# Kernel optimization log

Measured on AMD Instinct MI355X. Metric: run time of the kernel, lower is better.

Reference implementation:

```python
import jax, jax.numpy as jnp
import numpy as np
from jax import lax

RADII = (0.1, 0.2, 0.4)
NSAMPLES = (16, 32, 128)
MLPS = ((3, 32, 32, 64), (3, 64, 64, 128), (3, 64, 96, 128))  # divide_ratio=1


def fps(xyz, npoint):
    # iterative farthest point sampling; xyz [B,N,3] -> idx [B,npoint]
    B, N, _ = xyz.shape
    def body(carry, _):
        mind, last = carry
        p = jnp.take_along_axis(xyz, last[:, None, None], axis=1)  # [B,1,3]
        d = jnp.sum((xyz - p) ** 2, -1)
        mind = jnp.minimum(mind, d)
        nxt = jnp.argmax(mind, -1).astype(jnp.int32)
        return (mind, nxt), last
    init = (jnp.full((B, N), 1e10, xyz.dtype), jnp.zeros((B,), jnp.int32))
    _, idx = lax.scan(body, init, None, length=npoint)
    return jnp.transpose(idx)  # [B,npoint]


def ball_query(radius, nsample, xyz, new_xyz):
    # first-nsample neighbors within radius; pad with first valid index
    N = xyz.shape[1]
    sq = jnp.sum((new_xyz[:, :, None, :] - xyz[:, None, :, :]) ** 2, -1)  # [B,S,N]
    cand = jnp.where(sq < radius * radius,
                     jnp.arange(N, dtype=jnp.int32)[None, None, :], N)
    idx = jnp.sort(cand, axis=-1)[:, :, :nsample]
    first = idx[:, :, :1]
    return jnp.where(idx == N, first, idx).astype(jnp.int32)


def scale_branch(xyz, new_xyz, radius, nsample, weights):
    idx = ball_query(radius, nsample, xyz, new_xyz)
    grouped = jax.vmap(lambda x, i: x[i])(xyz, idx)          # [B,S,ns,3]
    h = grouped - new_xyz[:, :, None, :]                      # relative coords (points=None)
    for w, b in weights:                                      # shared 1x1-conv MLP
        h = jax.nn.relu(jnp.einsum('bsnc,co->bsno', h, w) + b)
    return jnp.max(h, axis=2)                                 # maxpool over neighbors [B,S,C]


def _forward(pcd, params, wf, bf):
    npoint = pcd.shape[1] // 8
    idx = fps(pcd, npoint)
    new_xyz = jnp.take_along_axis(pcd, idx[:, :, None], axis=1)  # [B,S,3]
    feats = [scale_branch(pcd, new_xyz, RADII[i], NSAMPLES[i], params[i]) for i in range(3)]
    h = jnp.concatenate(feats, axis=-1)                          # [B,S,320]
    return jnp.einsum('bsc,co->bso', h, wf) + bf                 # patch values [B,S,1]


def setup_inputs() -> dict:
    key = jax.random.key(0)
    ks = jax.random.split(key, 32)
    B, N = 8, 4096
    inp = {"pcd": jax.random.uniform(ks[0], (B, N, 3), jnp.float32)}
    ki = 1
    for si, dims in enumerate(MLPS):
        for li in range(3):
            cin, cout = dims[li], dims[li + 1]
            inp[f"w{si}{li}"] = jax.random.normal(ks[ki], (cin, cout), jnp.float32) * (2.0 / cin) ** 0.5
            inp[f"b{si}{li}"] = jnp.zeros((cout,), jnp.float32)
            ki += 1
    inp["wf"] = jax.random.normal(ks[ki], (320, 1), jnp.float32) * 0.05
    inp["bf"] = jnp.zeros((1,), jnp.float32)
    return inp


def reference(pcd, w00, b00, w01, b01, w02, b02,
              w10, b10, w11, b11, w12, b12,
              w20, b20, w21, b21, w22, b22, wf, bf):
    params = [[(w00, b00), (w01, b01), (w02, b02)],
              [(w10, b10), (w11, b11), (w12, b12)],
              [(w20, b20), (w21, b21), (w22, b22)]]
    return _forward(pcd, params, wf, bf)
```

## Files before the change

kernel.cpp:

```cpp
#include <hip/hip_runtime.h>

#define BATCH 8
#define NPTS 4096
#define NSAMP 512

#define ROW_SHR(n) (0x110 | (n))
#define ROW_BCAST15 0x142
#define ROW_BCAST31 0x143

typedef __attribute__((ext_vector_type(8))) short bf16x8;
typedef __attribute__((ext_vector_type(4))) float f32x4;

__device__ __forceinline__ unsigned short f2bf(float f) {
  unsigned u = __float_as_uint(f);
  unsigned r = (u + 0x7FFFu + ((u >> 16) & 1u)) >> 16;
  return (unsigned short)r;
}
__device__ __forceinline__ float bf2f(unsigned short h) {
  return __uint_as_float(((unsigned)h) << 16);
}

template <int CTRL, int RMASK>
__device__ __forceinline__ float fmax_dpp(float x) {
  int t = __builtin_amdgcn_update_dpp(0, __float_as_int(x), CTRL, RMASK, 0xf, true);
  return fmaxf(x, __int_as_float(t));
}

__device__ __forceinline__ float wave_max(float x) {
  x = fmax_dpp<ROW_SHR(1), 0xf>(x);
  x = fmax_dpp<ROW_SHR(2), 0xf>(x);
  x = fmax_dpp<ROW_SHR(4), 0xf>(x);
  x = fmax_dpp<ROW_SHR(8), 0xf>(x);
  x = fmax_dpp<ROW_BCAST15, 0xa>(x);
  x = fmax_dpp<ROW_BCAST31, 0xc>(x);
  return x;
}

__device__ __forceinline__ void tsec(int g, const float* __restrict__ w,
                                     float* __restrict__ wt, int cin, int cinp,
                                     int cout, int base) {
  int local = g - base;
  if (local < 0 || local >= cinp * cout) return;
  int oc = local / cinp, ic = local % cinp;
  wt[base + local] = (ic < cin) ? w[ic * cout + oc] : 0.0f;
}

__device__ __forceinline__ void rowpack(int g, const float* __restrict__ w20,
                                        const float* __restrict__ b20,
                                        const float* __restrict__ w21,
                                        float* __restrict__ wt, int base) {
  int local = g - base;
  if (local < 0 || local >= 4 * 64 * 32) return;
  int wq = local / (64 * 32);
  int r = local % (64 * 32);
  int k = r / 32, j = r % 32;
  float v;
  if (j < 3) v = w20[j * 64 + k];
  else if (j == 3) v = b20[k];
  else if (j < 28) v = w21[k * 96 + wq * 24 + (j - 4)];
  else v = 0.0f;
  wt[base + local] = v;
}

__device__ __forceinline__ void awfill(int g, const float* __restrict__ w22,
                                       unsigned short* __restrict__ aw,
                                       int base) {
  int id = g - base;
  if (id < 0 || id >= 12288) return;
  int e = id & 7;
  int l = (id >> 3) & 63;
  int bq = id >> 9;
  int ot = bq / 3, ks = bq % 3;
  int oc = ot * 16 + (l & 15);
  int k = ks * 32 + (l >> 4) * 8 + e;
  float v = w22[k * 128 + oc];
  unsigned short h = f2bf(v);
  unsigned short lo = f2bf(__fsub_rn(v, bf2f(h)));
  aw[(bq * 64 + l) * 16 + e] = h;
  aw[(bq * 64 + l) * 16 + 8 + e] = lo;
}

#define W00 0
#define W01 128
#define W02 1152
#define W10 3200
#define W11 3456
#define W12 7552
#define WROW 15744
#define AWID 23936
#define ID_TOTAL 36224

__global__ __launch_bounds__(256) void prep_kernel(
    const float* w00, const float* w01, const float* w02,
    const float* w10, const float* w11, const float* w12,
    const float* w20, const float* b20, const float* w21, const float* w22,
    float* __restrict__ wt, unsigned short* __restrict__ aw) {
  int g = blockIdx.x * 256 + threadIdx.x;
  tsec(g, w00, wt, 3, 4, 32, W00);
  tsec(g, w01, wt, 32, 32, 32, W01);
  tsec(g, w02, wt, 32, 32, 64, W02);
  tsec(g, w10, wt, 3, 4, 64, W10);
  tsec(g, w11, wt, 64, 64, 64, W11);
  tsec(g, w12, wt, 64, 64, 128, W12);
  rowpack(g, w20, b20, w21, wt, WROW);
  awfill(g, w22, aw, AWID);
}

template <int TOC, int TN>
__device__ __forceinline__ void ib(float (&acc)[TOC][TN], const float* bias) {
#pragma unroll
  for (int j = 0; j < TOC; ++j) {
    float bj = bias[j];
#pragma unroll
    for (int i = 0; i < TN; ++i) acc[j][i] = bj;
  }
}

template <int CIN4, int TOC, int TN, int NTPI, int WS>
__device__ __forceinline__ void layer_acc(const float* __restrict__ wtb,
                                          const float* hin,
                                          float (&acc)[TOC][TN], int tn) {
#pragma unroll 2
  for (int c4 = 0; c4 < CIN4; ++c4) {
    float hv[4][TN];
#pragma unroll
    for (int k = 0; k < 4; ++k) {
      const float* src = &hin[(c4 * 4 + k) * NTPI + tn * TN];
      if constexpr (TN == 1) {
        hv[k][0] = src[0];
      } else if constexpr (TN == 2) {
        float2 v = *(const float2*)src; hv[k][0] = v.x; hv[k][1] = v.y;
      } else {
        float4 v = *(const float4*)src;
        hv[k][0] = v.x; hv[k][1] = v.y; hv[k][2] = v.z; hv[k][3] = v.w;
      }
    }
#pragma unroll
    for (int j = 0; j < TOC; ++j) {
      float4 w4 = *(const float4*)&wtb[j * WS + c4 * 4];
#pragma unroll
      for (int i = 0; i < TN; ++i) {
        acc[j][i] = fmaf(hv[0][i], w4.x, acc[j][i]);
        acc[j][i] = fmaf(hv[1][i], w4.y, acc[j][i]);
        acc[j][i] = fmaf(hv[2][i], w4.z, acc[j][i]);
        acc[j][i] = fmaf(hv[3][i], w4.w, acc[j][i]);
      }
    }
  }
}

template <int TOC, int TN, int NTPO>
__device__ __forceinline__ void store_relu(float* hout,
                                           float (&acc)[TOC][TN], int tn) {
#pragma unroll
  for (int j = 0; j < TOC; ++j) {
    float* dst = &hout[j * NTPO + tn * TN];
    if constexpr (TN == 1) {
      dst[0] = fmaxf(acc[j][0], 0.0f);
    } else if constexpr (TN == 2) {
      *(float2*)dst = make_float2(fmaxf(acc[j][0], 0.0f),
                                  fmaxf(acc[j][1], 0.0f));
    } else {
      *(float4*)dst = make_float4(fmaxf(acc[j][0], 0.0f),
                                  fmaxf(acc[j][1], 0.0f),
                                  fmaxf(acc[j][2], 0.0f),
                                  fmaxf(acc[j][3], 0.0f));
    }
  }
}

template <int TOC, int TN>
__device__ __forceinline__ float rmax_dot(const float* wfp,
                                          float (&acc)[TOC][TN], int tn) {
  float s = 0.0f;
#pragma unroll
  for (int j = 0; j < TOC; ++j) {
    float v = 0.0f;
#pragma unroll
    for (int i = 0; i < TN; ++i) v = fmaxf(v, acc[j][i]);
    v = fmaxf(v, __shfl_xor(v, 1));
    v = fmaxf(v, __shfl_xor(v, 2));
    v = fmaxf(v, __shfl_xor(v, 4));
    v = fmaxf(v, __shfl_xor(v, 8));
    if (tn == 0) s = fmaf(v, wfp[j], s);
  }
  return s;
}

__global__ __launch_bounds__(256) void fused_kernel(
    const float* __restrict__ pcd, float* __restrict__ new_xyz,
    int* __restrict__ ctrl, const float* __restrict__ wt,
    const unsigned short* __restrict__ aw,
    const float* __restrict__ b00, const float* __restrict__ b01,
    const float* __restrict__ b02, const float* __restrict__ b10,
    const float* __restrict__ b11, const float* __restrict__ b12,
    const float* __restrict__ b21, const float* __restrict__ b22,
    const float* __restrict__ wf, const float* __restrict__ bf,
    float* __restrict__ out) {
  __shared__ __align__(16) float lds[6160];

  const int tid = threadIdx.x;
  int* progress = ctrl + 8;

  if (tid == 0) ((int*)lds)[0] = atomicAdd(&ctrl[0], 1);
  __syncthreads();
  const int ticket = ((int*)lds)[0];

  if (ticket < BATCH) {
    const int b = ticket;
    const int t = tid;
    const int wave = t >> 6, lane = t & 63;
    const float* xb = pcd + (size_t)b * NPTS * 3;
    float4* slot = (float4*)(lds + 16);

    float X[16], Y[16], Z[16], mind[16];
    {
      float f[48];
      float4* vv = (float4*)f;
      const float4* src = (const float4*)xb + t * 12;
#pragma unroll
      for (int q = 0; q < 12; ++q) vv[q] = src[q];
#pragma unroll
      for (int j = 0; j < 16; ++j) {
        X[j] = f[3 * j + 0]; Y[j] = f[3 * j + 1]; Z[j] = f[3 * j + 2];
        mind[j] = 10000000000.0f;
      }
    }
    float px = xb[0], py = xb[1], pz = xb[2];

    for (int it = 0; it < NSAMP; ++it) {
      if (t == 0) {
        int* dst = (int*)(new_xyz + ((size_t)b * NSAMP + it) * 3);
        atomicExch(&dst[0], __float_as_int(px));
        atomicExch(&dst[1], __float_as_int(py));
        atomicExch(&dst[2], __float_as_int(pz));
        if ((it & 7) == 7)
          __hip_atomic_store(&progress[b], it + 1, __ATOMIC_RELEASE,
                             __HIP_MEMORY_SCOPE_AGENT);
      }
      float bv = -1.0f, bx = 0.0f, by = 0.0f, bz = 0.0f;
#pragma unroll
      for (int j = 0; j < 16; ++j) {
        float dx = __fsub_rn(X[j], px);
        float dy = __fsub_rn(Y[j], py);
        float dz = __fsub_rn(Z[j], pz);
        float d = __fadd_rn(__fadd_rn(__fmul_rn(dx, dx), __fmul_rn(dy, dy)),
                            __fmul_rn(dz, dz));
        float m = fminf(mind[j], d);
        mind[j] = m;
        bool g = m > bv;
        bv = g ? m : bv;
        bx = g ? X[j] : bx; by = g ? Y[j] : by; bz = g ? Z[j] : bz;
      }
      float wmax = __int_as_float(
          __builtin_amdgcn_readlane(__float_as_int(wave_max(bv)), 63));
      unsigned long long msk = __ballot(bv == wmax);
      if (lane == __ffsll(msk) - 1)
        slot[(it & 1) * 4 + wave] = make_float4(bx, by, bz, wmax);
      __syncthreads();
      float4 cur = slot[(it & 1) * 4 + 0];
#pragma unroll
      for (int w = 1; w < 4; ++w) {
        float4 sw = slot[(it & 1) * 4 + w];
        if (sw.w > cur.w) cur = sw;
      }
      px = cur.x; py = cur.y; pz = cur.z;
    }
    return;
  }

  const int tk = ticket - BATCH;
  const int b = tk & 7;
  const int s = tk >> 3;
  const int bs = (b << 9) | s;
  const int lane = tid & 63;
  const int wave = tid >> 6;
  const int tn = tid & 15, toc = tid >> 4;
  const float* xb = pcd + (size_t)b * NPTS * 3;

  float* bc = lds + 4;
  float* wsum = lds + 8;
  char* h2b = (char*)(lds + 16);
  unsigned long long* masks = (unsigned long long*)(lds + 16);
  unsigned short* gl = (unsigned short*)(lds + 400);
  float* cbuf = lds + 488;
  float* sB = lds + 760;
  float* sA = lds + 2936;

  if (tid == 0) {
    while (__hip_atomic_load(&progress[b], __ATOMIC_ACQUIRE,
                             __HIP_MEMORY_SCOPE_AGENT) <= s)
      __builtin_amdgcn_s_sleep(2);
    const int* src = (const int*)(new_xyz + (size_t)bs * 3);
    bc[0] = __int_as_float(__hip_atomic_load(&src[0], __ATOMIC_RELAXED,
                                             __HIP_MEMORY_SCOPE_AGENT));
    bc[1] = __int_as_float(__hip_atomic_load(&src[1], __ATOMIC_RELAXED,
                                             __HIP_MEMORY_SCOPE_AGENT));
    bc[2] = __int_as_float(__hip_atomic_load(&src[2], __ATOMIC_RELAXED,
                                             __HIP_MEMORY_SCOPE_AGENT));
  }
  __syncthreads();
  const float cx = bc[0], cy = bc[1], cz = bc[2];

  const float r2a = (float)(0.1 * 0.1);
  const float r2b = (float)(0.2 * 0.2);
  const float r2c = (float)(0.4 * 0.4);
#pragma unroll 4
  for (int j = 0; j < 16; ++j) {
    int i = (j << 8) | tid;
    const float* p = xb + i * 3;
    float dx = __fsub_rn(cx, p[0]);
    float dy = __fsub_rn(cy, p[1]);
    float dz = __fsub_rn(cz, p[2]);
    float sq = __fadd_rn(__fadd_rn(__fmul_rn(dx, dx), __fmul_rn(dy, dy)),
                         __fmul_rn(dz, dz));
    unsigned long long m0 = __ballot(sq < r2a);
    unsigned long long m1 = __ballot(sq < r2b);
    unsigned long long m2 = __ballot(sq < r2c);
    if (lane == 0) {
      int c = (j << 2) | wave;
      masks[0 * 64 + c] = m0; masks[1 * 64 + c] = m1; masks[2 * 64 + c] = m2;
    }
  }
  __syncthreads();

  if (wave < 3) {
    const int ns  = (wave == 0) ? 16 : (wave == 1) ? 32 : 128;
    const int off = (wave == 0) ? 0  : (wave == 1) ? 16 : 48;
    unsigned long long m = masks[wave * 64 + lane];
    int pc = (int)__popcll(m);
    int incl = pc;
#pragma unroll
    for (int o = 1; o < 64; o <<= 1) {
      int u = __shfl_up(incl, o);
      if (lane >= o) incl += u;
    }
    int ex = incl - pc;
    int total = __shfl(incl, 63);
    unsigned short* glw = gl + off;
    unsigned long long mm = m;
    int p = ex;
    while (mm && p < ns) {
      int l = (int)__builtin_ctzll(mm);
      mm &= mm - 1;
      glw[p++] = (unsigned short)((lane << 6) | l);
    }
    int cnt = total < ns ? total : ns;
    unsigned long long nz = __ballot(pc > 0);
    int fl = __ffsll(nz) - 1;
    int myf = (lane << 6) | (int)__builtin_ctzll(m | 0x8000000000000000ull);
    int fidx = __shfl(myf, fl);
    for (int k = cnt + lane; k < ns; k += 64) glw[k] = (unsigned short)fidx;
  }
  __syncthreads();

  const int gi0 = gl[48 + lane];
  const int gi1 = gl[112 + lane];
  if (tid < 68) cbuf[3 * 68 + tid] = 0.0f;
  if (tid < 48) {
    int j = gl[tid];
    const float* p = xb + 3 * j;
    cbuf[0 * 68 + tid] = __fsub_rn(p[0], cx);
    cbuf[1 * 68 + tid] = __fsub_rn(p[1], cy);
    cbuf[2 * 68 + tid] = __fsub_rn(p[2], cz);
  }
  const float* q0 = xb + 3 * gi0;
  const float* q1 = xb + 3 * gi1;
  const float dx0 = __fsub_rn(q0[0], cx);
  const float dy0 = __fsub_rn(q0[1], cy);
  const float dz0 = __fsub_rn(q0[2], cz);
  const float dx1 = __fsub_rn(q1[0], cx);
  const float dy1 = __fsub_rn(q1[1], cy);
  const float dz1 = __fsub_rn(q1[2], cz);
  __syncthreads();

  const int wq = __builtin_amdgcn_readfirstlane(wave);
  float dot = 0.0f;

  {
    float a[2][1]; ib<2, 1>(a, b00 + toc * 2);
    layer_acc<1, 2, 1, 68, 4>(wt + W00 + (toc * 2) * 4, cbuf, a, tn);
    store_relu<2, 1, 18>(sB + (toc * 2) * 18, a, tn);
  }
  __syncthreads();

  {
    float a[2][1]; ib<2, 1>(a, b01 + toc * 2);
    layer_acc<8, 2, 1, 18, 32>(wt + W01 + (toc * 2) * 32, sB, a, tn);
    store_relu<2, 1, 18>(sA + (toc * 2) * 18, a, tn);
  }
  __syncthreads();

  {
    float a[4][1]; ib<4, 1>(a, b02 + toc * 4);
    layer_acc<8, 4, 1, 18, 32>(wt + W02 + (toc * 4) * 32, sA, a, tn);
    dot += rmax_dot<4, 1>(wf + toc * 4, a, tn);
    float a1[4][2]; ib<4, 2>(a1, b10 + toc * 4);
    layer_acc<1, 4, 2, 68, 4>(wt + W10 + (toc * 4) * 4, cbuf + 16, a1, tn);
    store_relu<4, 2, 34>(sB + (toc * 4) * 34, a1, tn);
  }
  __syncthreads();

  {
    float a[4][2]; ib<4, 2>(a, b11 + toc * 4);
    layer_acc<16, 4, 2, 34, 64>(wt + W11 + (toc * 4) * 64, sB, a, tn);
    store_relu<4, 2, 34>(sA + (toc * 4) * 34, a, tn);
  }
  __syncthreads();

  {
    float a[8][2]; ib<8, 2>(a, b12 + toc * 8);
    layer_acc<16, 8, 2, 34, 64>(wt + W12 + (toc * 8) * 64, sA, a, tn);
    dot += rmax_dot<8, 2>(wf + 64 + toc * 8, a, tn);
  }
  __syncthreads();

  float rm2[8];
#pragma unroll
  for (int j = 0; j < 8; ++j) rm2[j] = 0.0f;
  const int fq = lane >> 4, fr = lane & 15;

#pragma unroll 1
  for (int pass = 0; pass < 2; ++pass) {
    const float pdx = pass ? dx1 : dx0;
    const float pdy = pass ? dy1 : dy0;
    const float pdz = pass ? dz1 : dz0;

    {
      const float* wp = wt + WROW + wq * 2048;
      const float* bp = b21 + wq * 24;
      float acc[24];
#pragma unroll
      for (int j = 0; j < 24; ++j) acc[j] = bp[j];
#pragma unroll 4
      for (int k = 0; k < 64; ++k) {
        const float* row = wp + k * 32;
        float a2 = row[3];
        a2 = fmaf(pdx, row[0], a2);
        a2 = fmaf(pdy, row[1], a2);
        a2 = fmaf(pdz, row[2], a2);
        float hv = fmaxf(a2, 0.0f);
#pragma unroll
        for (int j = 0; j < 24; ++j) acc[j] = fmaf(hv, row[4 + j], acc[j]);
      }
      char* hb = h2b + lane * 384;
      const int nx = lane & 7;
#pragma unroll
      for (int c = 0; c < 3; ++c) {
        int ph[4], pl[4];
#pragma unroll
        for (int q = 0; q < 4; ++q) {
          float a0 = fmaxf(acc[c * 8 + 2 * q], 0.0f);
          float a1 = fmaxf(acc[c * 8 + 2 * q + 1], 0.0f);
          unsigned short h0 = f2bf(a0);
          unsigned short l0 = f2bf(__fsub_rn(a0, bf2f(h0)));
          unsigned short h1 = f2bf(a1);
          unsigned short l1 = f2bf(__fsub_rn(a1, bf2f(h1)));
          ph[q] = (int)((unsigned)h0 | ((unsigned)h1 << 16));
          pl[q] = (int)((unsigned)l0 | ((unsigned)l1 << 16));
        }
        const int g = 6 * wq + 2 * c;
        *(int4*)(hb + ((g ^ nx) << 4)) = make_int4(ph[0], ph[1], ph[2], ph[3]);
        *(int4*)(hb + (((g + 1) ^ nx) << 4)) =
            make_int4(pl[0], pl[1], pl[2], pl[3]);
      }
    }
    __syncthreads();

    {
      f32x4 C[2][4];
#pragma unroll
      for (int i = 0; i < 2; ++i) {
        float bv[4];
#pragma unroll
        for (int r = 0; r < 4; ++r)
          bv[r] = b22[(wq * 2 + i) * 16 + fq * 4 + r];
#pragma unroll
        for (int t = 0; t < 4; ++t)
#pragma unroll
          for (int r = 0; r < 4; ++r) C[i][t][r] = bv[r];
      }
#pragma unroll
      for (int ks = 0; ks < 3; ++ks) {
        bf16x8 Ah[2], Al[2];
#pragma unroll
        for (int i = 0; i < 2; ++i) {
          const unsigned short* ab =
              aw + (((wq * 2 + i) * 3 + ks) * 64 + lane) * 16;
          Ah[i] = *(const bf16x8*)ab;
          Al[i] = *(const bf16x8*)(ab + 8);
        }
        const int kc = ks * 4 + fq;
#pragma unroll
        for (int t = 0; t < 4; ++t) {
          const int n = t * 16 + fr, nx = n & 7;
          const char* nb = h2b + n * 384;
          bf16x8 Bh = *(const bf16x8*)(nb + (((2 * kc) ^ nx) << 4));
          bf16x8 Bl = *(const bf16x8*)(nb + (((2 * kc + 1) ^ nx) << 4));
#pragma unroll
          for (int i = 0; i < 2; ++i) {
            C[i][t] = __builtin_amdgcn_mfma_f32_16x16x32_bf16(
                Ah[i], Bh, C[i][t], 0, 0, 0);
            C[i][t] = __builtin_amdgcn_mfma_f32_16x16x32_bf16(
                Ah[i], Bl, C[i][t], 0, 0, 0);
            C[i][t] = __builtin_amdgcn_mfma_f32_16x16x32_bf16(
                Al[i], Bh, C[i][t], 0, 0, 0);
          }
        }
      }
#pragma unroll
      for (int i = 0; i < 2; ++i)
#pragma unroll
        for (int t = 0; t < 4; ++t)
#pragma unroll
          for (int r = 0; r < 4; ++r)
            rm2[i * 4 + r] = fmaxf(rm2[i * 4 + r], fmaxf(C[i][t][r], 0.0f));
    }
    __syncthreads();
  }

#pragma unroll
  for (int i = 0; i < 2; ++i)
#pragma unroll
    for (int r = 0; r < 4; ++r) {
      float v = rm2[i * 4 + r];
      v = fmaxf(v, __shfl_xor(v, 1));
      v = fmaxf(v, __shfl_xor(v, 2));
      v = fmaxf(v, __shfl_xor(v, 4));
      v = fmaxf(v, __shfl_xor(v, 8));
      if (fr == 0)
        dot = fmaf(v, wf[192 + (wq * 2 + i) * 16 + fq * 4 + r], dot);
    }

#pragma unroll
  for (int o = 1; o < 64; o <<= 1) dot += __shfl_xor(dot, o);
  if (lane == 0) wsum[wq] = dot;
  __syncthreads();
  if (tid == 0)
    out[bs] = wsum[0] + wsum[1] + wsum[2] + wsum[3] + bf[0];
}

extern "C" void kernel_launch(void* const* d_in, const int* in_sizes, int n_in,
                              void* d_out, int out_size, void* d_ws, size_t ws_size,
                              hipStream_t stream) {
  const float* pcd = (const float*)d_in[0];
  float* wsf = (float*)d_ws;
  float* new_xyz = wsf;
  float* wt = wsf + 12288;
  unsigned short* aw = (unsigned short*)(wsf + 36224);
  int* ctrl = (int*)(wsf + 48512);

  hipMemsetAsync(ctrl, 0, 64, stream);

  prep_kernel<<<(ID_TOTAL + 255) / 256, 256, 0, stream>>>(
      (const float*)d_in[1], (const float*)d_in[3], (const float*)d_in[5],
      (const float*)d_in[7], (const float*)d_in[9], (const float*)d_in[11],
      (const float*)d_in[13], (const float*)d_in[14], (const float*)d_in[15],
      (const float*)d_in[17], wt, aw);

  fused_kernel<<<BATCH * NSAMP + BATCH, 256, 0, stream>>>(
      pcd, new_xyz, ctrl, wt, aw,
      (const float*)d_in[2],  (const float*)d_in[4],  (const float*)d_in[6],
      (const float*)d_in[8],  (const float*)d_in[10], (const float*)d_in[12],
      (const float*)d_in[16], (const float*)d_in[18],
      (const float*)d_in[19], (const float*)d_in[20],
      (float*)d_out);
}
```

Before: 483.9 us.

## Move scale-2 layer-2 matmul to split-bf16 MFMA and overlap stage passes

The 64->96 second layer of the largest-radius branch used to be a scalar FMA loop per lane. It now runs on MFMA with hi/lo bf16 splitting, using weights pre-packed by the prep kernel. The first layer's output is written to a swizzled LDS buffer, and the two 64-neighbour passes are interleaved so one pass's h1 computation overlaps the other's layer-3 MFMAs. LDS use per block rises from about 24KB to 40KB, which may reduce occupancy, and the bf16 split adds a small precision risk.

Result: slower. 521.3 us (+7.7%).

```diff
diff --git a/kernel.cpp b/kernel.cpp
--- a/kernel.cpp
+++ b/kernel.cpp
@@ -45,26 +45,36 @@
   wt[base + local] = (ic < cin) ? w[ic * cout + oc] : 0.0f;
 }
 
-__device__ __forceinline__ void rowpack(int g, const float* __restrict__ w20,
-                                        const float* __restrict__ b20,
-                                        const float* __restrict__ w21,
-                                        float* __restrict__ wt, int base) {
+__device__ __forceinline__ void rowpack4(int g, const float* __restrict__ w20,
+                                         const float* __restrict__ b20,
+                                         float* __restrict__ wt, int base) {
   int local = g - base;
-  if (local < 0 || local >= 4 * 64 * 32) return;
-  int wq = local / (64 * 32);
-  int r = local % (64 * 32);
-  int k = r / 32, j = r % 32;
-  float v;
-  if (j < 3) v = w20[j * 64 + k];
-  else if (j == 3) v = b20[k];
-  else if (j < 28) v = w21[k * 96 + wq * 24 + (j - 4)];
-  else v = 0.0f;
-  wt[base + local] = v;
-}
-
-__device__ __forceinline__ void awfill(int g, const float* __restrict__ w22,
-                                       unsigned short* __restrict__ aw,
-                                       int base) {
+  if (local < 0 || local >= 256) return;
+  int k = local >> 2, j = local & 3;
+  wt[base + local] = (j < 3) ? w20[j * 64 + k] : b20[k];
+}
+
+__device__ __forceinline__ void awfill21(int g, const float* __restrict__ w21,
+                                         unsigned short* __restrict__ aw,
+                                         int base) {
+  int id = g - base;
+  if (id < 0 || id >= 6144) return;
+  int e = id & 7;
+  int l = (id >> 3) & 63;
+  int fi = id >> 9;
+  int ot = fi >> 1, ks = fi & 1;
+  int oc = ot * 16 + (l & 15);
+  int k = ks * 32 + (l >> 4) * 8 + e;
+  float v = w21[k * 96 + oc];
+  unsigned short h = f2bf(v);
+  unsigned short lo = f2bf(__fsub_rn(v, bf2f(h)));
+  aw[(fi * 64 + l) * 16 + e] = h;
+  aw[(fi * 64 + l) * 16 + 8 + e] = lo;
+}
+
+__device__ __forceinline__ void awfill22(int g, const float* __restrict__ w22,
+                                         unsigned short* __restrict__ aw,
+                                         int base) {
   int id = g - base;
   if (id < 0 || id >= 12288) return;
   int e = id & 7;
@@ -76,8 +86,8 @@
   float v = w22[k * 128 + oc];
   unsigned short h = f2bf(v);
   unsigned short lo = f2bf(__fsub_rn(v, bf2f(h)));
-  aw[(bq * 64 + l) * 16 + e] = h;
-  aw[(bq * 64 + l) * 16 + 8 + e] = lo;
+  aw[12288 + (bq * 64 + l) * 16 + e] = h;
+  aw[12288 + (bq * 64 + l) * 16 + 8 + e] = lo;
 }
 
 #define W00 0
@@ -86,9 +96,10 @@
 #define W10 3200
 #define W11 3456
 #define W12 7552
-#define WROW 15744
-#define AWID 23936
-#define ID_TOTAL 36224
+#define WR4 15744
+#define AW21ID 16000
+#define AW22ID 22144
+#define ID_TOTAL 34432
 
 __global__ __launch_bounds__(256) void prep_kernel(
     const float* w00, const float* w01, const float* w02,
@@ -102,8 +113,9 @@
   tsec(g, w10, wt, 3, 4, 64, W10);
   tsec(g, w11, wt, 64, 64, 64, W11);
   tsec(g, w12, wt, 64, 64, 128, W12);
-  rowpack(g, w20, b20, w21, wt, WROW);
-  awfill(g, w22, aw, AWID);
+  rowpack4(g, w20, b20, wt, WR4);
+  awfill21(g, w21, aw, AW21ID);
+  awfill22(g, w22, aw, AW22ID);
 }
 
 template <int TOC, int TN>
@@ -187,6 +199,136 @@
   return s;
 }
 
+__device__ __forceinline__ void h1_stage(const float* __restrict__ wr4,
+                                         float pdx, float pdy, float pdz,
+                                         int lane, int wq, char* h1b) {
+  float hv[16];
+#pragma unroll
+  for (int kk = 0; kk < 16; ++kk) {
+    const float* row = wr4 + (wq * 16 + kk) * 4;
+    float a2 = row[3];
+    a2 = fmaf(pdx, row[0], a2);
+    a2 = fmaf(pdy, row[1], a2);
+    a2 = fmaf(pdz, row[2], a2);
+    hv[kk] = fmaxf(a2, 0.0f);
+  }
+  char* hb = h1b + lane * 256;
+  const int nx = lane & 7;
+#pragma unroll
+  for (int c = 0; c < 2; ++c) {
+    int ph[4], pl[4];
+#pragma unroll
+    for (int q = 0; q < 4; ++q) {
+      float a0 = hv[c * 8 + 2 * q], a1 = hv[c * 8 + 2 * q + 1];
+      unsigned short h0 = f2bf(a0);
+      unsigned short l0 = f2bf(__fsub_rn(a0, bf2f(h0)));
+      unsigned short h1v = f2bf(a1);
+      unsigned short l1 = f2bf(__fsub_rn(a1, bf2f(h1v)));
+      ph[q] = (int)((unsigned)h0 | ((unsigned)h1v << 16));
+      pl[q] = (int)((unsigned)l0 | ((unsigned)l1 << 16));
+    }
+    const int g = (wq * 2 + c) * 2;
+    *(int4*)(hb + ((g ^ nx) << 4)) = make_int4(ph[0], ph[1], ph[2], ph[3]);
+    *(int4*)(hb + (((g + 1) ^ nx) << 4)) =
+        make_int4(pl[0], pl[1], pl[2], pl[3]);
+  }
+}
+
+__device__ __forceinline__ void l21_mfma(const unsigned short* __restrict__ aw,
+                                         const float* __restrict__ b21,
+                                         const char* h1b, char* h2b,
+                                         int lane, int wq) {
+  const int fq = lane >> 4, fr = lane & 15;
+  const int n = wq * 16 + fr, nx = n & 7;
+  const char* nb = h1b + n * 256;
+  bf16x8 Bh[2], Bl[2];
+#pragma unroll
+  for (int ks = 0; ks < 2; ++ks) {
+    const int kc = ks * 4 + fq;
+    Bh[ks] = *(const bf16x8*)(nb + (((kc * 2) ^ nx) << 4));
+    Bl[ks] = *(const bf16x8*)(nb + (((kc * 2 + 1) ^ nx) << 4));
+  }
+  char* ob = h2b + n * 384;
+#pragma unroll
+  for (int ot = 0; ot < 6; ++ot) {
+    f32x4 C;
+#pragma unroll
+    for (int r = 0; r < 4; ++r) C[r] = b21[ot * 16 + fq * 4 + r];
+#pragma unroll
+    for (int ks = 0; ks < 2; ++ks) {
+      const unsigned short* ab = aw + ((ot * 2 + ks) * 64 + lane) * 16;
+      bf16x8 Ah = *(const bf16x8*)ab;
+      bf16x8 Al = *(const bf16x8*)(ab + 8);
+      C = __builtin_amdgcn_mfma_f32_16x16x32_bf16(Ah, Bh[ks], C, 0, 0, 0);
+      C = __builtin_amdgcn_mfma_f32_16x16x32_bf16(Ah, Bl[ks], C, 0, 0, 0);
+      C = __builtin_amdgcn_mfma_f32_16x16x32_bf16(Al, Bh[ks], C, 0, 0, 0);
+    }
+    int ph[2], pl[2];
+#pragma unroll
+    for (int q = 0; q < 2; ++q) {
+      float a0 = fmaxf(C[2 * q], 0.0f), a1 = fmaxf(C[2 * q + 1], 0.0f);
+      unsigned short h0 = f2bf(a0), l0 = f2bf(__fsub_rn(a0, bf2f(h0)));
+      unsigned short h1v = f2bf(a1), l1 = f2bf(__fsub_rn(a1, bf2f(h1v)));
+      ph[q] = (int)((unsigned)h0 | ((unsigned)h1v << 16));
+      pl[q] = (int)((unsigned)l0 | ((unsigned)l1 << 16));
+    }
+    const int kc2 = ot * 2 + (fq >> 1);
+    const int sub = (fq & 1) * 8;
+    *(int2*)(ob + (((kc2 * 2) ^ nx) << 4) + sub) = make_int2(ph[0], ph[1]);
+    *(int2*)(ob + (((kc2 * 2 + 1) ^ nx) << 4) + sub) = make_int2(pl[0], pl[1]);
+  }
+}
+
+__device__ __forceinline__ void l22_mfma(const unsigned short* __restrict__ aw,
+                                         const float* __restrict__ b22,
+                                         const char* h2b, int lane, int wq,
+                                         float (&rm2)[8]) {
+  const int fq = lane >> 4, fr = lane & 15;
+  f32x4 C[2][4];
+#pragma unroll
+  for (int i = 0; i < 2; ++i) {
+    float bv[4];
+#pragma unroll
+    for (int r = 0; r < 4; ++r) bv[r] = b22[(wq * 2 + i) * 16 + fq * 4 + r];
+#pragma unroll
+    for (int t = 0; t < 4; ++t)
+#pragma unroll
+      for (int r = 0; r < 4; ++r) C[i][t][r] = bv[r];
+  }
+#pragma unroll
+  for (int ks = 0; ks < 3; ++ks) {
+    bf16x8 Ah[2], Al[2];
+#pragma unroll
+    for (int i = 0; i < 2; ++i) {
+      const unsigned short* ab =
+          aw + 12288 + (((wq * 2 + i) * 3 + ks) * 64 + lane) * 16;
+      Ah[i] = *(const bf16x8*)ab;
+      Al[i] = *(const bf16x8*)(ab + 8);
+    }
+    const int kc = ks * 4 + fq;
+#pragma unroll
+    for (int t = 0; t < 4; ++t) {
+      const int n = t * 16 + fr, nx = n & 7;
+      const char* nb = h2b + n * 384;
+      bf16x8 Bh = *(const bf16x8*)(nb + (((2 * kc) ^ nx) << 4));
+      bf16x8 Bl = *(const bf16x8*)(nb + (((2 * kc + 1) ^ nx) << 4));
+#pragma unroll
+      for (int i = 0; i < 2; ++i) {
+        C[i][t] = __builtin_amdgcn_mfma_f32_16x16x32_bf16(Ah[i], Bh, C[i][t], 0, 0, 0);
+        C[i][t] = __builtin_amdgcn_mfma_f32_16x16x32_bf16(Ah[i], Bl, C[i][t], 0, 0, 0);
+        C[i][t] = __builtin_amdgcn_mfma_f32_16x16x32_bf16(Al[i], Bh, C[i][t], 0, 0, 0);
+      }
+    }
+  }
+#pragma unroll
+  for (int i = 0; i < 2; ++i)
+#pragma unroll
+    for (int t = 0; t < 4; ++t)
+#pragma unroll
+      for (int r = 0; r < 4; ++r)
+        rm2[i * 4 + r] = fmaxf(rm2[i * 4 + r], fmaxf(C[i][t][r], 0.0f));
+}
+
 __global__ __launch_bounds__(256) void fused_kernel(
     const float* __restrict__ pcd, float* __restrict__ new_xyz,
     int* __restrict__ ctrl, const float* __restrict__ wt,
@@ -197,7 +339,7 @@
     const float* __restrict__ b21, const float* __restrict__ b22,
     const float* __restrict__ wf, const float* __restrict__ bf,
     float* __restrict__ out) {
-  __shared__ __align__(16) float lds[6160];
+  __shared__ __align__(16) float lds[10240];
 
   const int tid = threadIdx.x;
   int* progress = ctrl + 8;
@@ -278,14 +420,15 @@
   const int tn = tid & 15, toc = tid >> 4;
   const float* xb = pcd + (size_t)b * NPTS * 3;
 
+  char* h2b = (char*)lds;
+  char* h1b = (char*)(lds + 6144);
   float* bc = lds + 4;
-  float* wsum = lds + 8;
-  char* h2b = (char*)(lds + 16);
-  unsigned long long* masks = (unsigned long long*)(lds + 16);
-  unsigned short* gl = (unsigned short*)(lds + 400);
-  float* cbuf = lds + 488;
-  float* sB = lds + 760;
-  float* sA = lds + 2936;
+  float* sB = lds + 16;
+  float* sA = lds + 2192;
+  unsigned long long* masks = (unsigned long long*)(lds + 6144);
+  unsigned short* gl = (unsigned short*)(lds + 6528);
+  float* cbuf = lds + 6616;
+  float* wsum = lds + 6144;
 
   if (tid == 0) {
     while (__hip_atomic_load(&progress[b], __ATOMIC_ACQUIRE,
@@ -375,6 +518,7 @@
   __syncthreads();
 
   const int wq = __builtin_amdgcn_readfirstlane(wave);
+  const float* wr4 = wt + WR4;
   float dot = 0.0f;
 
   {
@@ -409,6 +553,7 @@
   __syncthreads();
 
   {
+    h1_stage(wr4, dx0, dy0, dz0, lane, wq, h1b);
     float a[8][2]; ib<8, 2>(a, b12 + toc * 8);
     layer_acc<16, 8, 2, 34, 64>(wt + W12 + (toc * 8) * 64, sA, a, tn);
     dot += rmax_dot<8, 2>(wf + 64 + toc * 8, a, tn);
@@ -420,105 +565,17 @@
   for (int j = 0; j < 8; ++j) rm2[j] = 0.0f;
   const int fq = lane >> 4, fr = lane & 15;
 
-#pragma unroll 1
-  for (int pass = 0; pass < 2; ++pass) {
-    const float pdx = pass ? dx1 : dx0;
-    const float pdy = pass ? dy1 : dy0;
-    const float pdz = pass ? dz1 : dz0;
-
-    {
-      const float* wp = wt + WROW + wq * 2048;
-      const float* bp = b21 + wq * 24;
-      float acc[24];
-#pragma unroll
-      for (int j = 0; j < 24; ++j) acc[j] = bp[j];
-#pragma unroll 4
-      for (int k = 0; k < 64; ++k) {
-        const float* row = wp + k * 32;
-        float a2 = row[3];
-        a2 = fmaf(pdx, row[0], a2);
-        a2 = fmaf(pdy, row[1], a2);
-        a2 = fmaf(pdz, row[2], a2);
-        float hv = fmaxf(a2, 0.0f);
-#pragma unroll
-        for (int j = 0; j < 24; ++j) acc[j] = fmaf(hv, row[4 + j], acc[j]);
-      }
-      char* hb = h2b + lane * 384;
-      const int nx = lane & 7;
-#pragma unroll
-      for (int c = 0; c < 3; ++c) {
-        int ph[4], pl[4];
-#pragma unroll
-        for (int q = 0; q < 4; ++q) {
-          float a0 = fmaxf(acc[c * 8 + 2 * q], 0.0f);
-          float a1 = fmaxf(acc[c * 8 + 2 * q + 1], 0.0f);
-          unsigned short h0 = f2bf(a0);
-          unsigned short l0 = f2bf(__fsub_rn(a0, bf2f(h0)));
-          unsigned short h1 = f2bf(a1);
-          unsigned short l1 = f2bf(__fsub_rn(a1, bf2f(h1)));
-          ph[q] = (int)((unsigned)h0 | ((unsigned)h1 << 16));
-          pl[q] = (int)((unsigned)l0 | ((unsigned)l1 << 16));
-        }
-        const int g = 6 * wq + 2 * c;
-        *(int4*)(hb + ((g ^ nx) << 4)) = make_int4(ph[0], ph[1], ph[2], ph[3]);
-        *(int4*)(hb + (((g + 1) ^ nx) << 4)) =
-            make_int4(pl[0], pl[1], pl[2], pl[3]);
-      }
-    }
-    __syncthreads();
-
-    {
-      f32x4 C[2][4];
-#pragma unroll
-      for (int i = 0; i < 2; ++i) {
-        float bv[4];
-#pragma unroll
-        for (int r = 0; r < 4; ++r)
-          bv[r] = b22[(wq * 2 + i) * 16 + fq * 4 + r];
-#pragma unroll
-        for (int t = 0; t < 4; ++t)
-#pragma unroll
-          for (int r = 0; r < 4; ++r) C[i][t][r] = bv[r];
-      }
-#pragma unroll
-      for (int ks = 0; ks < 3; ++ks) {
-        bf16x8 Ah[2], Al[2];
-#pragma unroll
-        for (int i = 0; i < 2; ++i) {
-          const unsigned short* ab =
-              aw + (((wq * 2 + i) * 3 + ks) * 64 + lane) * 16;
-          Ah[i] = *(const bf16x8*)ab;
-          Al[i] = *(const bf16x8*)(ab + 8);
-        }
-        const int kc = ks * 4 + fq;
-#pragma unroll
-        for (int t = 0; t < 4; ++t) {
-          const int n = t * 16 + fr, nx = n & 7;
-          const char* nb = h2b + n * 384;
-          bf16x8 Bh = *(const bf16x8*)(nb + (((2 * kc) ^ nx) << 4));
-          bf16x8 Bl = *(const bf16x8*)(nb + (((2 * kc + 1) ^ nx) << 4));
-#pragma unroll
-          for (int i = 0; i < 2; ++i) {
-            C[i][t] = __builtin_amdgcn_mfma_f32_16x16x32_bf16(
-                Ah[i], Bh, C[i][t], 0, 0, 0);
-            C[i][t] = __builtin_amdgcn_mfma_f32_16x16x32_bf16(
-                Ah[i], Bl, C[i][t], 0, 0, 0);
-            C[i][t] = __builtin_amdgcn_mfma_f32_16x16x32_bf16(
-                Al[i], Bh, C[i][t], 0, 0, 0);
-          }
-        }
-      }
-#pragma unroll
-      for (int i = 0; i < 2; ++i)
-#pragma unroll
-        for (int t = 0; t < 4; ++t)
-#pragma unroll
-          for (int r = 0; r < 4; ++r)
-            rm2[i * 4 + r] = fmaxf(rm2[i * 4 + r], fmaxf(C[i][t][r], 0.0f));
-    }
-    __syncthreads();
-  }
-
+  l21_mfma(aw, b21, h1b, h2b, lane, wq);
+  __syncthreads();
+
+  h1_stage(wr4, dx1, dy1, dz1, lane, wq, h1b);
+  l22_mfma(aw, b22, h2b, lane, wq, rm2);
+  __syncthreads();
+
+  l21_mfma(aw, b21, h1b, h2b, lane, wq);
+  __syncthreads();
+
+  l22_mfma(aw, b22, h2b, lane, wq, rm2);
 #pragma unroll
   for (int i = 0; i < 2; ++i)
 #pragma unroll
@@ -547,8 +604,8 @@
   float* wsf = (float*)d_ws;
   float* new_xyz = wsf;
   float* wt = wsf + 12288;
-  unsigned short* aw = (unsigned short*)(wsf + 36224);
-  int* ctrl = (int*)(wsf + 48512);
+  unsigned short* aw = (unsigned short*)(wsf + 28288);
+  int* ctrl = (int*)(wsf + 46720);
 
   hipMemsetAsync(ctrl, 0, 64, stream);
 
```
